# Kernel tuning notes

Measured on AMD Instinct MI355X. Metric: run time of the kernel, lower is better.

Reference implementation:

```python
import jax, jax.numpy as jnp
import numpy as np

B, C, H, W, HEADS = 8, 256, 128, 128, 8
HEADC = C // HEADS
EPS = 1e-5


def _ln(t, w, b):
    # per-head LayerNorm over the head-channel dim (last axis),
    # with per-head affine params of shape (heads, 1, headc)
    mu = jnp.mean(t, axis=-1, keepdims=True)
    var = jnp.mean(jnp.square(t - mu), axis=-1, keepdims=True)
    return (t - mu) * jax.lax.rsqrt(var + EPS) * w + b


def _forward(x, w_qkv, b_qkv, kln_w, kln_b, vln_w, vln_b, w_o1, b_o1, w_o2, b_o2):
    b, c, h, w = x.shape
    n = h * w
    heads, headc = kln_w.shape[0], c // kln_w.shape[0]
    # 1x1 conv qkv projection, channels-last output: [b,h,w,3c]
    qkv = jnp.einsum('bchw,oc->bhwo', x, w_qkv) + b_qkv
    qkv = qkv.reshape(b, n, heads, 3 * headc).transpose(0, 2, 1, 3)  # [b,heads,n,3*headc]
    q, k, v = jnp.split(qkv, 3, axis=-1)  # each [b,heads,n,headc]
    k = _ln(k, kln_w, kln_b)
    v = _ln(v, vln_w, vln_b)
    # Galerkin linear attention: (k^T v) then q @ (k^T v), normalized by n
    kv = jnp.einsum('bhnd,bhne->bhde', k, v) / n  # [b,heads,headc,headc]
    att = jnp.einsum('bhnd,bhde->bhne', q, kv)    # [b,heads,n,headc]
    att = att.transpose(0, 2, 1, 3).reshape(b, h, w, c).transpose(0, 3, 1, 2)
    ret = att + x
    y = jnp.einsum('bchw,oc->bohw', ret, w_o1) + b_o1[None, :, None, None]
    y = jax.nn.gelu(y, approximate=False)  # torch nn.GELU default = exact erf
    y = jnp.einsum('bchw,oc->bohw', y, w_o2) + b_o2[None, :, None, None]
    return y + x


def setup_inputs() -> dict:
    key = jax.random.key(0)
    ks = jax.random.split(key, 4)
    return {
        'x': jax.random.normal(ks[0], (B, C, H, W), dtype=jnp.float32),
        'w_qkv': jax.random.normal(ks[1], (3 * C, C), dtype=jnp.float32) * 0.02,
        'b_qkv': jnp.zeros((3 * C,), dtype=jnp.float32),
        'kln_w': jnp.ones((HEADS, 1, HEADC), dtype=jnp.float32),
        'kln_b': jnp.zeros((HEADS, 1, HEADC), dtype=jnp.float32),
        'vln_w': jnp.ones((HEADS, 1, HEADC), dtype=jnp.float32),
        'vln_b': jnp.zeros((HEADS, 1, HEADC), dtype=jnp.float32),
        'w_o1': jax.random.normal(ks[2], (C, C), dtype=jnp.float32) * 0.02,
        'b_o1': jnp.zeros((C,), dtype=jnp.float32),
        'w_o2': jax.random.normal(ks[3], (C, C), dtype=jnp.float32) * 0.02,
        'b_o2': jnp.zeros((C,), dtype=jnp.float32),
    }


def reference(x, w_qkv, b_qkv, kln_w, kln_b, vln_w, vln_b, w_o1, b_o1, w_o2, b_o2):
    return _forward(x, w_qkv, b_qkv, kln_w, kln_b, vln_w, vln_b, w_o1, b_o1, w_o2, b_o2)
```

## Files before the change

kernel.cpp:

```cpp
#include <hip/hip_runtime.h>
#include <hip/hip_bf16.h>
#include <cstdint>

typedef unsigned short u16;
typedef __attribute__((ext_vector_type(8))) short short8;
typedef __attribute__((ext_vector_type(4))) short short4v;
typedef __attribute__((ext_vector_type(4))) float f32x4;

#define HW_N 16384
#define CCH  256
#define BATCH 8
#define NHEAD 8
#define HEADC 32

static __device__ __forceinline__ float bf2f(u16 u){
    union { float f; uint32_t i; } x; x.i = ((uint32_t)u) << 16; return x.f;
}
static __device__ __forceinline__ u16 f2bf(float f){
    union { float f; uint32_t i; } x; x.f = f;
    uint32_t r = x.i + 0x7fffu + ((x.i >> 16) & 1u);
    return (u16)(r >> 16);
}

#define GLD16(gp, lp) __builtin_amdgcn_global_load_lds( \
    (const __attribute__((address_space(1))) uint32_t*)(gp), \
    (__attribute__((address_space(3))) uint32_t*)(lp), 16, 0, 0)

__global__ __launch_bounds__(256) void k_transpose_cast(const float* __restrict__ x,
                                                        u16* __restrict__ xb){
    __shared__ float tile[64][65];
    int b = blockIdx.z, ct = blockIdx.y, nt = blockIdx.x;
    int t = threadIdx.x;
    const float* src = x + ((size_t)b * CCH + ct * 64) * HW_N + nt * 64;
    #pragma unroll
    for (int it = 0; it < 16; ++it){
        int f = it * 256 + t;
        int i = f >> 6, j = f & 63;
        tile[i][j] = src[(size_t)i * HW_N + j];
    }
    __syncthreads();
    u16* dst = xb + ((size_t)b * HW_N + nt * 64) * CCH + ct * 64;
    #pragma unroll
    for (int it = 0; it < 16; ++it){
        int f = it * 256 + t;
        int jj = f >> 6, ii = f & 63;
        dst[(size_t)jj * CCH + ii] = f2bf(tile[ii][jj]);
    }
}

__global__ __launch_bounds__(256) void k_weight_prep(const float* __restrict__ w_qkv,
                                                     const float* __restrict__ b_qkv,
                                                     const float* __restrict__ w_o1,
                                                     const float* __restrict__ w_o2,
                                                     u16* __restrict__ wkv_b,
                                                     float* __restrict__ bkv_re,
                                                     u16* __restrict__ w_o1_b,
                                                     u16* __restrict__ w_o2_b){
    int id = blockIdx.x * 256 + threadIdx.x;
    if (id < 512 * 256){
        int r = id >> 8, c = id & 255;
        int h = r >> 6, s = (r >> 5) & 1, d = r & 31;
        int srow = h * 96 + 32 + s * 32 + d;
        wkv_b[id] = f2bf(w_qkv[(size_t)srow * 256 + c]);
        if (c == 0) bkv_re[r] = b_qkv[srow];
    } else {
        int id2 = id - 512 * 256;
        if (id2 < 65536)       w_o1_b[id2]         = f2bf(w_o1[id2]);
        else if (id2 < 131072) w_o2_b[id2 - 65536] = f2bf(w_o2[id2 - 65536]);
    }
}

template<bool GELU, bool RESID, bool OUTF32>
__global__ __launch_bounds__(256, 4) void k_gemm(const u16* __restrict__ A,
                                                 const u16* __restrict__ Bt0,
                                                 const float* __restrict__ bias0,
                                                 const u16* __restrict__ resid,
                                                 u16* __restrict__ out,
                                                 const float* __restrict__ xres,
                                                 float* __restrict__ outf,
                                                 int NC, int Mb,
                                                 long bt_stride, int bias_stride){
    __shared__ __align__(16) u16 sh[16384];
    u16* lsA = sh;
    u16* lsB = sh + 8192;

    int gx = gridDim.x;
    int lin = blockIdx.x + gx * (blockIdx.y + gridDim.y * blockIdx.z);
    int lg = (gx == 4) ? 2 : 1;
    int bx = (lin >> 3) & (gx - 1);
    int rest = (lin & 7) | ((lin >> (3 + lg)) << 3);
    int by = rest & 127;
    int bz = rest >> 7;

    int row0 = bz * Mb + by * 128;
    int col0 = bx * 128;
    const u16* Bt = Bt0 + (size_t)bz * bt_stride;
    const float* bias = bias0 + (size_t)bz * bias_stride;

    int t = threadIdx.x;
    int wid = t >> 6, lane = t & 63;
    int wr = wid >> 1, wc = wid & 1;

    f32x4 acc[4][4];
    #pragma unroll
    for (int i = 0; i < 4; ++i)
        #pragma unroll
        for (int j = 0; j < 4; ++j) acc[i][j] = (f32x4)0.0f;

    for (int kt = 0; kt < 4; ++kt){
        int c0 = kt * 64;
        #pragma unroll
        for (int it = 0; it < 4; ++it){
            int f  = it * 256 + t;
            int fs = f ^ ((f >> 3) & 7);
            int r  = f >> 3, c8 = (fs & 7) * 8;
            GLD16(&A [((size_t)(row0 + r)) * 256 + c0 + c8], &lsA[f * 8]);
            GLD16(&Bt[((size_t)(col0 + r)) * 256 + c0 + c8], &lsB[f * 8]);
        }
        __syncthreads();
        int lrow = lane & 15;
        #pragma unroll
        for (int ks = 0; ks < 2; ++ks){
            int lk = (lane >> 4) * 8 + ks * 32;
            short8 af[4], bfr[4];
            #pragma unroll
            for (int mi = 0; mi < 4; ++mi){
                int row = wr * 64 + mi * 16 + lrow;
                int e = (row * 64 + lk) ^ ((row & 7) << 3);
                af[mi] = *(const short8*)&lsA[e];
            }
            #pragma unroll
            for (int ni = 0; ni < 4; ++ni){
                int row = wc * 64 + ni * 16 + lrow;
                int e = (row * 64 + lk) ^ ((row & 7) << 3);
                bfr[ni] = *(const short8*)&lsB[e];
            }
            #pragma unroll
            for (int mi = 0; mi < 4; ++mi)
                #pragma unroll
                for (int ni = 0; ni < 4; ++ni)
                    acc[mi][ni] = OUTF32
                        ? __builtin_amdgcn_mfma_f32_16x16x32_bf16(af[mi], bfr[ni], acc[mi][ni], 0, 0, 0)
                        : __builtin_amdgcn_mfma_f32_16x16x32_bf16(bfr[ni], af[mi], acc[mi][ni], 0, 0, 0);
        }
        __syncthreads();
    }

    {
        int lrow = lane & 15, q4 = (lane >> 4) * 4;
        #pragma unroll
        for (int mi = 0; mi < 4; ++mi){
            #pragma unroll
            for (int ni = 0; ni < 4; ++ni){
                short4v pk;
                #pragma unroll
                for (int r = 0; r < 4; ++r) pk[r] = (short)f2bf(acc[mi][ni][r]);
                int byteoff;
                if (!OUTF32){
                    int nloc = wr * 64 + mi * 16 + lrow;
                    int oloc = wc * 64 + ni * 16 + q4;
                    byteoff = (nloc << 8) + (oloc << 1);
                    byteoff ^= ((nloc ^ (nloc >> 2)) & 3) << 5;
                } else {
                    int oloc = wc * 64 + ni * 16 + lrow;
                    int nloc = wr * 64 + mi * 16 + q4;
                    byteoff = (oloc << 8) + (nloc << 1);
                    byteoff ^= (oloc & 15) << 4;
                }
                *(short4v*)((char*)sh + byteoff) = pk;
            }
        }
    }
    __syncthreads();

    if (!OUTF32){
        #pragma unroll
        for (int it = 0; it < 8; ++it){
            int f = it * 256 + t;
            int row = f >> 4, cb = f & 15;
            int byteoff = (row << 8) + ((cb << 4) ^ ((((row ^ (row >> 2)) & 3) << 5)));
            short8 av = *(const short8*)((char*)sh + byteoff);
            int gr = row0 + row;
            int gc = col0 + cb * 8;
            f32x4 bv0 = *(const f32x4*)&bias[gc];
            f32x4 bv1 = *(const f32x4*)&bias[gc + 4];
            float vv[8];
            #pragma unroll
            for (int j = 0; j < 4; ++j){ vv[j] = bf2f((u16)av[j]) + bv0[j];
                                         vv[j+4] = bf2f((u16)av[j+4]) + bv1[j]; }
            if (RESID){
                short8 rv = *(const short8*)&resid[(size_t)gr * NC + gc];
                #pragma unroll
                for (int j = 0; j < 8; ++j) vv[j] += bf2f((u16)rv[j]);
            }
            if (GELU){
                #pragma unroll
                for (int j = 0; j < 8; ++j)
                    vv[j] = 0.5f * vv[j] * (1.0f + erff(vv[j] * 0.70710678118654752f));
            }
            short8 pk;
            #pragma unroll
            for (int j = 0; j < 8; ++j) pk[j] = (short)f2bf(vv[j]);
            *(short8*)&out[(size_t)gr * NC + gc] = pk;
        }
    } else {
        #pragma unroll
        for (int it = 0; it < 8; ++it){
            int f = it * 256 + t;
            int o = f >> 4, nb = f & 15;
            int byteoff = (o << 8) + ((nb ^ (o & 15)) << 4);
            short8 av = *(const short8*)((char*)sh + byteoff);
            int go = col0 + o;
            size_t base = ((size_t)(bz * 256 + go)) * HW_N + by * 128 + nb * 8;
            float bo = bias[go];
            f32x4 x0 = *(const f32x4*)&xres[base];
            f32x4 x1 = *(const f32x4*)&xres[base + 4];
            f32x4 o0, o1;
            #pragma unroll
            for (int j = 0; j < 4; ++j){
                o0[j] = bf2f((u16)av[j])   + bo + x0[j];
                o1[j] = bf2f((u16)av[j+4]) + bo + x1[j];
            }
            *(f32x4*)&outf[base]     = o0;
            *(f32x4*)&outf[base + 4] = o1;
        }
    }
}

__global__ __launch_bounds__(256, 2) void k_gemm_kv(const u16* __restrict__ A,
                                                    const u16* __restrict__ Bt,
                                                    const float* __restrict__ bkv,
                                                    const float* __restrict__ kln_w,
                                                    const float* __restrict__ kln_b,
                                                    const float* __restrict__ vln_w,
                                                    const float* __restrict__ vln_b,
                                                    float* __restrict__ kvpart){
    __shared__ __align__(16) u16 sh[16384];
    u16* lsA = sh;
    u16* lsB = sh + 8192;

    int lin = blockIdx.x + 4 * (blockIdx.y + 128 * blockIdx.z);
    int bx = (lin >> 3) & 3;
    int rest = (lin & 7) | ((lin >> 5) << 3);
    int by = rest & 127;
    int bz = rest >> 7;

    int row0 = bz * HW_N + by * 128;
    int col0 = bx * 128;

    int t = threadIdx.x;
    int wid = t >> 6, lane = t & 63;
    int wr = wid >> 1, wc = wid & 1;
    int q = lane >> 4, q4 = q * 4, lrow = lane & 15;

    f32x4 acc[4][4];
    #pragma unroll
    for (int i = 0; i < 4; ++i)
        #pragma unroll
        for (int j = 0; j < 4; ++j) acc[i][j] = (f32x4)0.0f;

    for (int kt = 0; kt < 4; ++kt){
        int c0 = kt * 64;
        #pragma unroll
        for (int it = 0; it < 4; ++it){
            int f  = it * 256 + t;
            int fs = f ^ ((f >> 3) & 7);
            int r  = f >> 3, c8 = (fs & 7) * 8;
            GLD16(&A [((size_t)(row0 + r)) * 256 + c0 + c8], &lsA[f * 8]);
            GLD16(&Bt[((size_t)(col0 + r)) * 256 + c0 + c8], &lsB[f * 8]);
        }
        __syncthreads();
        #pragma unroll
        for (int ks = 0; ks < 2; ++ks){
            int lk = q * 8 + ks * 32;
            short8 af[4], bfr[4];
            #pragma unroll
            for (int mi = 0; mi < 4; ++mi){
                int row = wr * 64 + mi * 16 + lrow;
                int e = (row * 64 + lk) ^ ((row & 7) << 3);
                af[mi] = *(const short8*)&lsA[e];
            }
            #pragma unroll
            for (int ni = 0; ni < 4; ++ni){
                int row = wc * 64 + ni * 16 + lrow;
                int e = (row * 64 + lk) ^ ((row & 7) << 3);
                bfr[ni] = *(const short8*)&lsB[e];
            }
            #pragma unroll
            for (int mi = 0; mi < 4; ++mi)
                #pragma unroll
                for (int ni = 0; ni < 4; ++ni)
                    acc[mi][ni] = __builtin_amdgcn_mfma_f32_16x16x32_bf16(
                        bfr[ni], af[mi], acc[mi][ni], 0, 0, 0);
        }
        __syncthreads();
    }

    int h = 2 * bx + wc;
    float bv[4][4], lwv[4][4], lbv[4][4];
    #pragma unroll
    for (int ni = 0; ni < 4; ++ni){
        const float* w  = (ni < 2) ? kln_w : vln_w;
        const float* bb = (ni < 2) ? kln_b : vln_b;
        #pragma unroll
        for (int r = 0; r < 4; ++r){
            int de = (ni & 1) * 16 + q4 + r;
            bv[ni][r]  = bkv[col0 + wc * 64 + ni * 16 + q4 + r];
            lwv[ni][r] = w[h * 32 + de];
            lbv[ni][r] = bb[h * 32 + de];
        }
    }

    #pragma unroll
    for (int mi = 0; mi < 4; ++mi){
        float ks = 0.f, ksq = 0.f, vs = 0.f, vsq = 0.f;
        #pragma unroll
        for (int ni = 0; ni < 4; ++ni)
            #pragma unroll
            for (int r = 0; r < 4; ++r){
                float t2 = acc[mi][ni][r] + bv[ni][r];
                acc[mi][ni][r] = t2;
                if (ni < 2){ ks += t2; ksq += t2 * t2; }
                else       { vs += t2; vsq += t2 * t2; }
            }
        ks  += __shfl_xor(ks, 16);  ks  += __shfl_xor(ks, 32);
        ksq += __shfl_xor(ksq, 16); ksq += __shfl_xor(ksq, 32);
        vs  += __shfl_xor(vs, 16);  vs  += __shfl_xor(vs, 32);
        vsq += __shfl_xor(vsq, 16); vsq += __shfl_xor(vsq, 32);
        float muk = ks * 0.03125f, muv = vs * 0.03125f;
        float rsk = rsqrtf(fmaxf(ksq * 0.03125f - muk * muk, 0.f) + 1e-5f);
        float rsv = rsqrtf(fmaxf(vsq * 0.03125f - muv * muv, 0.f) + 1e-5f);
        int n = wr * 64 + mi * 16 + lrow;
        #pragma unroll
        for (int ni = 0; ni < 4; ++ni){
            float mu = (ni < 2) ? muk : muv;
            float rs = (ni < 2) ? rsk : rsv;
            #pragma unroll
            for (int r = 0; r < 4; ++r){
                int d = (ni & 1) * 16 + q4 + r;
                float val = (acc[mi][ni][r] - mu) * rs * lwv[ni][r] + lbv[ni][r];
                int byteoff = ((wc * 2 + (ni >> 1)) << 13) + (d << 8) + (n << 1);
                byteoff ^= (d & 7) << 4;
                *(u16*)((char*)sh + byteoff) = f2bf(val);
            }
        }
    }
    __syncthreads();

    if (wid < 2){
        f32x4 a2[2][2];
        #pragma unroll
        for (int i = 0; i < 2; ++i)
            #pragma unroll
            for (int j = 0; j < 2; ++j) a2[i][j] = (f32x4)0.0f;
        #pragma unroll
        for (int ks2 = 0; ks2 < 4; ++ks2){
            int n0 = q * 8 + ks2 * 32;
            short8 kf[2], vf[2];
            #pragma unroll
            for (int mi = 0; mi < 2; ++mi){
                int d = mi * 16 + lrow;
                int bko = ((wid * 2 + 0) << 13) + (d << 8) + (n0 << 1);
                int bvo = ((wid * 2 + 1) << 13) + (d << 8) + (n0 << 1);
                bko ^= (d & 7) << 4;
                bvo ^= (d & 7) << 4;
                kf[mi] = *(const short8*)((char*)sh + bko);
                vf[mi] = *(const short8*)((char*)sh + bvo);
            }
            #pragma unroll
            for (int mi = 0; mi < 2; ++mi)
                #pragma unroll
                for (int ni = 0; ni < 2; ++ni)
                    a2[mi][ni] = __builtin_amdgcn_mfma_f32_16x16x32_bf16(
                        kf[mi], vf[ni], a2[mi][ni], 0, 0, 0);
        }
        float* dst = kvpart + (((size_t)(bz * 128 + by)) * 8 + 2 * bx + wid) * 1024;
        #pragma unroll
        for (int mi = 0; mi < 2; ++mi)
            #pragma unroll
            for (int ni = 0; ni < 2; ++ni)
                #pragma unroll
                for (int r = 0; r < 4; ++r)
                    dst[(mi * 16 + q4 + r) * 32 + ni * 16 + lrow] = a2[mi][ni][r];
    }
}

__global__ __launch_bounds__(256) void k_wqeff(const float* __restrict__ kvpart,
                                               const float* __restrict__ w_qkv,
                                               const float* __restrict__ b_qkv,
                                               u16* __restrict__ wq_eff_b,
                                               float* __restrict__ beff){
    __shared__ float kv[1024];
    int h = blockIdx.x, b = blockIdx.y;
    int t = threadIdx.x;
    f32x4 s = (f32x4)0.0f;
    for (int p = 0; p < 128; ++p){
        f32x4 v = *(const f32x4*)(kvpart + (((size_t)b * 128 + p) * 8 + h) * 1024 + t * 4);
        s = s + v;
    }
    const float invN = 1.0f / (float)HW_N;
    #pragma unroll
    for (int i = 0; i < 4; ++i) kv[t * 4 + i] = s[i] * invN;
    __syncthreads();

    float wcol[32];
    #pragma unroll
    for (int d = 0; d < 32; ++d)
        wcol[d] = w_qkv[((size_t)(h * 96 + d)) * 256 + t];
    for (int e = 0; e < 32; ++e){
        float s2 = 0.f;
        #pragma unroll
        for (int d = 0; d < 32; ++d) s2 += wcol[d] * kv[d * 32 + e];
        wq_eff_b[(((size_t)b * 256) + h * 32 + e) * 256 + t] = f2bf(s2);
    }
    if (t < 32){
        float s3 = 0.f;
        #pragma unroll
        for (int d = 0; d < 32; ++d) s3 += b_qkv[h * 96 + d] * kv[d * 32 + t];
        beff[b * 256 + h * 32 + t] = s3;
    }
}

extern "C" void kernel_launch(void* const* d_in, const int* in_sizes, int n_in,
                              void* d_out, int out_size, void* d_ws, size_t ws_size,
                              hipStream_t stream){
    const float* x     = (const float*)d_in[0];
    const float* w_qkv = (const float*)d_in[1];
    const float* b_qkv = (const float*)d_in[2];
    const float* kln_w = (const float*)d_in[3];
    const float* kln_b = (const float*)d_in[4];
    const float* vln_w = (const float*)d_in[5];
    const float* vln_b = (const float*)d_in[6];
    const float* w_o1  = (const float*)d_in[7];
    const float* b_o1  = (const float*)d_in[8];
    const float* w_o2  = (const float*)d_in[9];
    const float* b_o2  = (const float*)d_in[10];
    float* out = (float*)d_out;

    const size_t MB = 1u << 20;
    if (ws_size < 266 * MB) return;

    char* ws = (char*)d_ws;
    u16*   xb      = (u16*)(ws);
    u16*   y1b     = (u16*)(ws + 64 * MB);
    float* kvpart  = (float*)(ws + 192 * MB);
    u16*   ret_b   = (u16*)(ws + 192 * MB);
    char*  sm      = ws + 264 * MB;
    u16*   wkv_b   = (u16*)sm;
    float* bkv_re  = (float*)(sm + 256 * 1024);
    u16*   w_o1_b  = (u16*)(sm + 260 * 1024);
    u16*   w_o2_b  = (u16*)(sm + 392 * 1024);
    u16*   wq_effb = (u16*)(sm + 524 * 1024);
    float* beff    = (float*)(sm + 1572 * 1024);

    k_transpose_cast<<<dim3(HW_N / 64, CCH / 64, BATCH), 256, 0, stream>>>(x, xb);
    k_weight_prep<<<dim3(1024), 256, 0, stream>>>(w_qkv, b_qkv, w_o1, w_o2,
                                                  wkv_b, bkv_re, w_o1_b, w_o2_b);
    k_gemm_kv<<<dim3(4, 128, BATCH), 256, 0, stream>>>(
        xb, wkv_b, bkv_re, kln_w, kln_b, vln_w, vln_b, kvpart);
    k_wqeff<<<dim3(NHEAD, BATCH), 256, 0, stream>>>(kvpart, w_qkv, b_qkv, wq_effb, beff);
    k_gemm<false, true, false><<<dim3(2, 128, BATCH), 256, 0, stream>>>(
        xb, wq_effb, beff, xb, ret_b, nullptr, nullptr, 256, HW_N, 65536, 256);
    k_gemm<true, false, false><<<dim3(2, 128, BATCH), 256, 0, stream>>>(
        ret_b, w_o1_b, b_o1, nullptr, y1b, nullptr, nullptr, 256, HW_N, 0, 0);
    k_gemm<false, false, true><<<dim3(2, 128, BATCH), 256, 0, stream>>>(
        y1b, w_o2_b, b_o2, nullptr, nullptr, x, out, 256, HW_N, 0, 0);
}
```

Measured before the change: 271.9 us.

## Fuse attention-apply, MLP1+GELU and MLP2 GEMMs into one kernel

Replaces three separate 128x128-tile GEMM launches with one kernel that holds a 64-row activation tile (all 256 channels) in LDS across three chained GEMMs. The intermediates (ret and GELU output) stay in shared memory and are never written to or read back from global memory. Weights are streamed through double-buffered LDS in 32-wide K slices. This removes the global round trips for the two bf16 intermediates and two launches. In exchange each weight matrix is reloaded per 64-row tile, LDS use rises to 64 KB per block (two blocks per CU), and a barrier follows every K step.

```diff
diff --git a/kernel.cpp b/kernel.cpp
--- a/kernel.cpp
+++ b/kernel.cpp
@@ -70,163 +70,6 @@
     }
 }
 
-template<bool GELU, bool RESID, bool OUTF32>
-__global__ __launch_bounds__(256, 4) void k_gemm(const u16* __restrict__ A,
-                                                 const u16* __restrict__ Bt0,
-                                                 const float* __restrict__ bias0,
-                                                 const u16* __restrict__ resid,
-                                                 u16* __restrict__ out,
-                                                 const float* __restrict__ xres,
-                                                 float* __restrict__ outf,
-                                                 int NC, int Mb,
-                                                 long bt_stride, int bias_stride){
-    __shared__ __align__(16) u16 sh[16384];
-    u16* lsA = sh;
-    u16* lsB = sh + 8192;
-
-    int gx = gridDim.x;
-    int lin = blockIdx.x + gx * (blockIdx.y + gridDim.y * blockIdx.z);
-    int lg = (gx == 4) ? 2 : 1;
-    int bx = (lin >> 3) & (gx - 1);
-    int rest = (lin & 7) | ((lin >> (3 + lg)) << 3);
-    int by = rest & 127;
-    int bz = rest >> 7;
-
-    int row0 = bz * Mb + by * 128;
-    int col0 = bx * 128;
-    const u16* Bt = Bt0 + (size_t)bz * bt_stride;
-    const float* bias = bias0 + (size_t)bz * bias_stride;
-
-    int t = threadIdx.x;
-    int wid = t >> 6, lane = t & 63;
-    int wr = wid >> 1, wc = wid & 1;
-
-    f32x4 acc[4][4];
-    #pragma unroll
-    for (int i = 0; i < 4; ++i)
-        #pragma unroll
-        for (int j = 0; j < 4; ++j) acc[i][j] = (f32x4)0.0f;
-
-    for (int kt = 0; kt < 4; ++kt){
-        int c0 = kt * 64;
-        #pragma unroll
-        for (int it = 0; it < 4; ++it){
-            int f  = it * 256 + t;
-            int fs = f ^ ((f >> 3) & 7);
-            int r  = f >> 3, c8 = (fs & 7) * 8;
-            GLD16(&A [((size_t)(row0 + r)) * 256 + c0 + c8], &lsA[f * 8]);
-            GLD16(&Bt[((size_t)(col0 + r)) * 256 + c0 + c8], &lsB[f * 8]);
-        }
-        __syncthreads();
-        int lrow = lane & 15;
-        #pragma unroll
-        for (int ks = 0; ks < 2; ++ks){
-            int lk = (lane >> 4) * 8 + ks * 32;
-            short8 af[4], bfr[4];
-            #pragma unroll
-            for (int mi = 0; mi < 4; ++mi){
-                int row = wr * 64 + mi * 16 + lrow;
-                int e = (row * 64 + lk) ^ ((row & 7) << 3);
-                af[mi] = *(const short8*)&lsA[e];
-            }
-            #pragma unroll
-            for (int ni = 0; ni < 4; ++ni){
-                int row = wc * 64 + ni * 16 + lrow;
-                int e = (row * 64 + lk) ^ ((row & 7) << 3);
-                bfr[ni] = *(const short8*)&lsB[e];
-            }
-            #pragma unroll
-            for (int mi = 0; mi < 4; ++mi)
-                #pragma unroll
-                for (int ni = 0; ni < 4; ++ni)
-                    acc[mi][ni] = OUTF32
-                        ? __builtin_amdgcn_mfma_f32_16x16x32_bf16(af[mi], bfr[ni], acc[mi][ni], 0, 0, 0)
-                        : __builtin_amdgcn_mfma_f32_16x16x32_bf16(bfr[ni], af[mi], acc[mi][ni], 0, 0, 0);
-        }
-        __syncthreads();
-    }
-
-    {
-        int lrow = lane & 15, q4 = (lane >> 4) * 4;
-        #pragma unroll
-        for (int mi = 0; mi < 4; ++mi){
-            #pragma unroll
-            for (int ni = 0; ni < 4; ++ni){
-                short4v pk;
-                #pragma unroll
-                for (int r = 0; r < 4; ++r) pk[r] = (short)f2bf(acc[mi][ni][r]);
-                int byteoff;
-                if (!OUTF32){
-                    int nloc = wr * 64 + mi * 16 + lrow;
-                    int oloc = wc * 64 + ni * 16 + q4;
-                    byteoff = (nloc << 8) + (oloc << 1);
-                    byteoff ^= ((nloc ^ (nloc >> 2)) & 3) << 5;
-                } else {
-                    int oloc = wc * 64 + ni * 16 + lrow;
-                    int nloc = wr * 64 + mi * 16 + q4;
-                    byteoff = (oloc << 8) + (nloc << 1);
-                    byteoff ^= (oloc & 15) << 4;
-                }
-                *(short4v*)((char*)sh + byteoff) = pk;
-            }
-        }
-    }
-    __syncthreads();
-
-    if (!OUTF32){
-        #pragma unroll
-        for (int it = 0; it < 8; ++it){
-            int f = it * 256 + t;
-            int row = f >> 4, cb = f & 15;
-            int byteoff = (row << 8) + ((cb << 4) ^ ((((row ^ (row >> 2)) & 3) << 5)));
-            short8 av = *(const short8*)((char*)sh + byteoff);
-            int gr = row0 + row;
-            int gc = col0 + cb * 8;
-            f32x4 bv0 = *(const f32x4*)&bias[gc];
-            f32x4 bv1 = *(const f32x4*)&bias[gc + 4];
-            float vv[8];
-            #pragma unroll
-            for (int j = 0; j < 4; ++j){ vv[j] = bf2f((u16)av[j]) + bv0[j];
-                                         vv[j+4] = bf2f((u16)av[j+4]) + bv1[j]; }
-            if (RESID){
-                short8 rv = *(const short8*)&resid[(size_t)gr * NC + gc];
-                #pragma unroll
-                for (int j = 0; j < 8; ++j) vv[j] += bf2f((u16)rv[j]);
-            }
-            if (GELU){
-                #pragma unroll
-                for (int j = 0; j < 8; ++j)
-                    vv[j] = 0.5f * vv[j] * (1.0f + erff(vv[j] * 0.70710678118654752f));
-            }
-            short8 pk;
-            #pragma unroll
-            for (int j = 0; j < 8; ++j) pk[j] = (short)f2bf(vv[j]);
-            *(short8*)&out[(size_t)gr * NC + gc] = pk;
-        }
-    } else {
-        #pragma unroll
-        for (int it = 0; it < 8; ++it){
-            int f = it * 256 + t;
-            int o = f >> 4, nb = f & 15;
-            int byteoff = (o << 8) + ((nb ^ (o & 15)) << 4);
-            short8 av = *(const short8*)((char*)sh + byteoff);
-            int go = col0 + o;
-            size_t base = ((size_t)(bz * 256 + go)) * HW_N + by * 128 + nb * 8;
-            float bo = bias[go];
-            f32x4 x0 = *(const f32x4*)&xres[base];
-            f32x4 x1 = *(const f32x4*)&xres[base + 4];
-            f32x4 o0, o1;
-            #pragma unroll
-            for (int j = 0; j < 4; ++j){
-                o0[j] = bf2f((u16)av[j])   + bo + x0[j];
-                o1[j] = bf2f((u16)av[j+4]) + bo + x1[j];
-            }
-            *(f32x4*)&outf[base]     = o0;
-            *(f32x4*)&outf[base + 4] = o1;
-        }
-    }
-}
-
 __global__ __launch_bounds__(256, 2) void k_gemm_kv(const u16* __restrict__ A,
                                                     const u16* __restrict__ Bt,
                                                     const float* __restrict__ bkv,
@@ -418,6 +261,147 @@
         #pragma unroll
         for (int d = 0; d < 32; ++d) s3 += b_qkv[h * 96 + d] * kv[d * 32 + t];
         beff[b * 256 + h * 32 + t] = s3;
+    }
+}
+
+#define STAGE_B(BT, KT, BUF) do {                                             \
+    _Pragma("unroll")                                                         \
+    for (int it_ = 0; it_ < 4; ++it_){                                        \
+        int f_ = it_ * 256 + t;                                               \
+        int o_ = f_ >> 2, sl_ = f_ & 3;                                       \
+        GLD16(&(BT)[(size_t)o_ * 256 + (KT) * 32 + (sl_ ^ (o_ & 3)) * 8],     \
+              &(BUF)[f_ * 8]);                                                \
+    }                                                                         \
+} while(0)
+
+#define ZACC do {                                                             \
+    _Pragma("unroll") for (int i_ = 0; i_ < 4; ++i_)                          \
+    _Pragma("unroll") for (int j_ = 0; j_ < 4; ++j_)                          \
+        acc[i_][j_] = (f32x4)0.0f;                                            \
+} while(0)
+
+#define KLOOP(BT, SWAPPED) do {                                               \
+    for (int kt = 0; kt < 8; ++kt){                                           \
+        int cur = kt & 1;                                                     \
+        if (kt < 7) STAGE_B(BT, kt + 1, Bs[cur ^ 1]);                         \
+        short8 af[4], bf[4];                                                  \
+        _Pragma("unroll")                                                     \
+        for (int mi = 0; mi < 4; ++mi){                                       \
+            int n_ = mi * 16 + lrow;                                          \
+            int sl_ = (kt * 4 + q) ^ (n_ & 7);                                \
+            af[mi] = *(const short8*)((const char*)I + n_ * 512 + (sl_ << 4));\
+        }                                                                     \
+        _Pragma("unroll")                                                     \
+        for (int ni = 0; ni < 4; ++ni){                                       \
+            int o_ = wid * 64 + ni * 16 + lrow;                               \
+            bf[ni] = *(const short8*)((const char*)Bs[cur] + o_ * 64          \
+                                      + ((q ^ (o_ & 3)) << 4));               \
+        }                                                                     \
+        _Pragma("unroll")                                                     \
+        for (int mi = 0; mi < 4; ++mi)                                        \
+            _Pragma("unroll")                                                 \
+            for (int ni = 0; ni < 4; ++ni)                                    \
+                acc[mi][ni] = (SWAPPED)                                       \
+                    ? __builtin_amdgcn_mfma_f32_16x16x32_bf16(                \
+                          bf[ni], af[mi], acc[mi][ni], 0, 0, 0)               \
+                    : __builtin_amdgcn_mfma_f32_16x16x32_bf16(                \
+                          af[mi], bf[ni], acc[mi][ni], 0, 0, 0);              \
+        __syncthreads();                                                      \
+    }                                                                         \
+} while(0)
+
+__global__ __launch_bounds__(256, 2) void k_fused3(const u16* __restrict__ xb,
+                                                   const u16* __restrict__ wq_effb,
+                                                   const float* __restrict__ beff,
+                                                   const u16* __restrict__ w_o1_b,
+                                                   const float* __restrict__ b_o1,
+                                                   const u16* __restrict__ w_o2_b,
+                                                   const float* __restrict__ b_o2,
+                                                   const float* __restrict__ x,
+                                                   float* __restrict__ out){
+    __shared__ __align__(16) u16 I[16384];
+    __shared__ __align__(16) u16 Bs[2][8192];
+
+    int d = blockIdx.x;
+    int bz = d & 7, nb = d >> 3;
+    size_t row0 = (size_t)bz * HW_N + (size_t)nb * 64;
+
+    int t = threadIdx.x, wid = t >> 6, lane = t & 63;
+    int lrow = lane & 15, q = lane >> 4, q4 = q * 4;
+
+    const u16* B1 = wq_effb + (size_t)bz * 65536;
+
+    #pragma unroll
+    for (int it = 0; it < 8; ++it){
+        int f = it * 256 + t;
+        int n = f >> 5, slot = f & 31;
+        GLD16(&xb[(row0 + n) * 256 + (size_t)((slot ^ (n & 7)) * 8)], &I[f * 8]);
+    }
+    STAGE_B(B1, 0, Bs[0]);
+    __syncthreads();
+
+    f32x4 acc[4][4];
+
+    ZACC;
+    KLOOP(B1, true);
+    STAGE_B(w_o1_b, 0, Bs[0]);
+    #pragma unroll
+    for (int ni = 0; ni < 4; ++ni){
+        int o0 = wid * 64 + ni * 16 + q4;
+        f32x4 be = *(const f32x4*)&beff[bz * 256 + o0];
+        #pragma unroll
+        for (int mi = 0; mi < 4; ++mi){
+            int n = mi * 16 + lrow;
+            int byte = (n * 512 + o0 * 2) ^ ((n & 7) << 4);
+            short4v rv = *(const short4v*)((const char*)I + byte);
+            short4v pk;
+            #pragma unroll
+            for (int r = 0; r < 4; ++r)
+                pk[r] = (short)f2bf(acc[mi][ni][r] + be[r] + bf2f((u16)rv[r]));
+            *(short4v*)((char*)I + byte) = pk;
+        }
+    }
+    __syncthreads();
+
+    ZACC;
+    KLOOP(w_o1_b, true);
+    STAGE_B(w_o2_b, 0, Bs[0]);
+    #pragma unroll
+    for (int ni = 0; ni < 4; ++ni){
+        int o0 = wid * 64 + ni * 16 + q4;
+        f32x4 bo = *(const f32x4*)&b_o1[o0];
+        #pragma unroll
+        for (int mi = 0; mi < 4; ++mi){
+            int n = mi * 16 + lrow;
+            int byte = (n * 512 + o0 * 2) ^ ((n & 7) << 4);
+            short4v pk;
+            #pragma unroll
+            for (int r = 0; r < 4; ++r){
+                float v = acc[mi][ni][r] + bo[r];
+                v = 0.5f * v * (1.0f + erff(v * 0.70710678118654752f));
+                pk[r] = (short)f2bf(v);
+            }
+            *(short4v*)((char*)I + byte) = pk;
+        }
+    }
+    __syncthreads();
+
+    ZACC;
+    KLOOP(w_o2_b, false);
+    #pragma unroll
+    for (int ni = 0; ni < 4; ++ni){
+        int o = wid * 64 + ni * 16 + lrow;
+        float bo = b_o2[o];
+        size_t base = ((size_t)bz * 256 + o) * HW_N + (size_t)nb * 64;
+        #pragma unroll
+        for (int mi = 0; mi < 4; ++mi){
+            int n0 = mi * 16 + q4;
+            f32x4 xv = *(const f32x4*)&x[base + n0];
+            f32x4 ov;
+            #pragma unroll
+            for (int r = 0; r < 4; ++r) ov[r] = acc[mi][ni][r] + bo + xv[r];
+            *(f32x4*)&out[base + n0] = ov;
+        }
     }
 }
 
@@ -442,9 +426,7 @@
 
     char* ws = (char*)d_ws;
     u16*   xb      = (u16*)(ws);
-    u16*   y1b     = (u16*)(ws + 64 * MB);
     float* kvpart  = (float*)(ws + 192 * MB);
-    u16*   ret_b   = (u16*)(ws + 192 * MB);
     char*  sm      = ws + 264 * MB;
     u16*   wkv_b   = (u16*)sm;
     float* bkv_re  = (float*)(sm + 256 * 1024);
@@ -459,10 +441,6 @@
     k_gemm_kv<<<dim3(4, 128, BATCH), 256, 0, stream>>>(
         xb, wkv_b, bkv_re, kln_w, kln_b, vln_w, vln_b, kvpart);
     k_wqeff<<<dim3(NHEAD, BATCH), 256, 0, stream>>>(kvpart, w_qkv, b_qkv, wq_effb, beff);
-    k_gemm<false, true, false><<<dim3(2, 128, BATCH), 256, 0, stream>>>(
-        xb, wq_effb, beff, xb, ret_b, nullptr, nullptr, 256, HW_N, 65536, 256);
-    k_gemm<true, false, false><<<dim3(2, 128, BATCH), 256, 0, stream>>>(
-        ret_b, w_o1_b, b_o1, nullptr, y1b, nullptr, nullptr, 256, HW_N, 0, 0);
-    k_gemm<false, false, true><<<dim3(2, 128, BATCH), 256, 0, stream>>>(
-        y1b, w_o2_b, b_o2, nullptr, nullptr, x, out, 256, HW_N, 0, 0);
-}
+    k_fused3<<<dim3(2048), 256, 0, stream>>>(
+        xb, wq_effb, beff, w_o1_b, b_o1, w_o2_b, b_o2, x, out);
+}
```

Measured after the change: 250.5 us. 7.9% less time.
